# Performance work log

Hardware: AMD Instinct MI355X
Metric: run time of the kernel (lower is better)

## Reference

```python
import jax, jax.numpy as jnp
import numpy as np

N = 50000        # nodes
E = 800000       # edges (avg degree 16)
F_IN = 128       # num_features
DIM = 128        # hidden dim
C = 10           # num_classes
TEMP = 0.6       # EntropyLinear default temperature
SLOPE = 0.01     # F.leaky_relu default negative slope


def setup_inputs() -> dict:
    key = jax.random.key(0)
    ks = jax.random.split(key, 12)
    x = jax.random.normal(ks[0], (N, F_IN), dtype=jnp.float32)
    edge_index = jax.random.randint(ks[1], (2, E), 0, N, dtype=jnp.int32)
    s_in = 1.0 / np.sqrt(F_IN)
    s_d = 1.0 / np.sqrt(DIM)
    W0 = jax.random.normal(ks[2], (F_IN, DIM), jnp.float32) * s_in
    b0 = jnp.zeros((DIM,), jnp.float32)
    W1 = jax.random.normal(ks[3], (DIM, DIM), jnp.float32) * s_d
    b1 = jnp.zeros((DIM,), jnp.float32)
    W2 = jax.random.normal(ks[4], (DIM, DIM), jnp.float32) * s_d
    b2 = jnp.zeros((DIM,), jnp.float32)
    W3 = jax.random.normal(ks[5], (DIM, DIM), jnp.float32) * s_d
    b3 = jnp.zeros((DIM,), jnp.float32)
    lens_w = jax.random.normal(ks[6], (C, 1, DIM), jnp.float32) * s_d  # (n_classes, out=1, in)
    lens_b = jax.random.normal(ks[7], (C, 1, 1), jnp.float32) * 0.01
    return dict(x=x, edge_index=edge_index, W0=W0, b0=b0, W1=W1, b1=b1,
                W2=W2, b2=b2, W3=W3, b3=b3, lens_w=lens_w, lens_b=lens_b)


def _gcn_conv(h, W, b, src, dst, norm):
    # PyG GCNConv: h' = scatter_add( norm_e * (h W)[src] ) + b
    m = h @ W                                  # [N, out]
    msg = m[src] * norm[:, None]               # [E+N, out] gather + scale
    agg = jax.ops.segment_sum(msg, dst, num_segments=N)
    return agg + b


def reference(x, edge_index, W0, b0, W1, b1, W2, b2, W3, b3, lens_w, lens_b):
    loops = jnp.arange(N, dtype=edge_index.dtype)
    src = jnp.concatenate([edge_index[0], loops])   # add self-loops
    dst = jnp.concatenate([edge_index[1], loops])
    deg = jax.ops.segment_sum(jnp.ones_like(dst, jnp.float32), dst, num_segments=N)
    dis = jnp.where(deg > 0, jax.lax.rsqrt(jnp.maximum(deg, 1.0)), 0.0)
    norm = dis[src] * dis[dst]                      # symmetric D^-1/2 A D^-1/2

    h = x
    for W, b in ((W0, b0), (W1, b1), (W2, b2), (W3, b3)):
        h = _gcn_conv(h, W, b, src, dst, norm)
        h = jax.nn.leaky_relu(h, SLOPE)

    p = jax.nn.softmax(h, axis=-1)
    concepts = p / jnp.max(p, axis=-1, keepdims=True)   # [N, DIM]

    # torch_explain EntropyLinear(DIM, 1, n_classes=C)
    gamma = jnp.abs(lens_w).sum(axis=1)                 # [C, DIM] L1 over out_features
    alpha = jax.nn.softmax(gamma / TEMP, axis=1)
    alpha_norm = alpha / jnp.max(alpha, axis=1, keepdims=True)
    z = concepts[None, :, :] * alpha_norm[:, None, :]   # [C, N, DIM]
    out = jnp.einsum('cnd,cod->cno', z, lens_w) + lens_b  # [C, N, 1]
    out = jnp.transpose(out, (1, 0, 2))                 # [N, C, 1]

    log_probs = jax.nn.log_softmax(out, axis=0).squeeze(-1)  # softmax over nodes
    return concepts, log_probs
```

## Files before the change

kernel.cpp:

```cpp
#include <hip/hip_runtime.h>


#define DIMF 128
#define GRID 1024
#define TPB  256

typedef __bf16 bf16x8 __attribute__((ext_vector_type(8)));
typedef float f32x4 __attribute__((ext_vector_type(4)));

static __device__ __forceinline__ ushort f2bf(float f) {
    uint u = __float_as_uint(f);
    u += 0x7fffu + ((u >> 16) & 1u);
    return (ushort)(u >> 16);
}
static __device__ __forceinline__ float bflo(uint u) { return __uint_as_float(u << 16); }
static __device__ __forceinline__ float bfhi(uint u) { return __uint_as_float(u & 0xffff0000u); }

static __device__ __forceinline__ void upadd(float* acc, const int4& u) {
    const uint* w = (const uint*)&u;
#pragma unroll
    for (int k = 0; k < 4; ++k) {
        acc[2 * k]     += bflo(w[k]);
        acc[2 * k + 1] += bfhi(w[k]);
    }
}


union SMem {
    ushort ws[16384];
    struct { int h[256]; } ha;
    struct { int tmp[256]; } sc;
    struct { int h[256]; int lb[256]; } sa;
    struct { int cnt[256]; int cur[256]; int tmp[256]; } pb;
    struct { float wcT[1280]; float lb[16]; } ep;
    struct { float2 red[4]; } r1;
    struct { float red[2]; } wc;
    struct { float2 red2[176]; float Ls[16]; } l3;
};


static __device__ __forceinline__ void gsync(uint* cb, uint r, uint& pop, uint xcc) {
    __syncthreads();
    if (threadIdx.x == 0) {
        uint* axc   = cb + 128 + 32 * xcc;
        uint* xdone = cb + 640 + 32 * xcc;
        uint* root  = cb + 32;
        if (pop == 0) {
            while (__hip_atomic_load(cb, __ATOMIC_RELAXED, __HIP_MEMORY_SCOPE_AGENT) < (uint)GRID)
                __builtin_amdgcn_s_sleep(2);
            pop = __hip_atomic_load(cb + 64 + xcc, __ATOMIC_RELAXED, __HIP_MEMORY_SCOPE_AGENT);
        }
        uint v = __hip_atomic_fetch_add(axc, 1u, __ATOMIC_RELAXED, __HIP_MEMORY_SCOPE_AGENT) + 1;
        if (v == r * pop) {
            __hip_atomic_fetch_add(root, pop, __ATOMIC_RELEASE, __HIP_MEMORY_SCOPE_AGENT);
            while (__hip_atomic_load(root, __ATOMIC_RELAXED, __HIP_MEMORY_SCOPE_AGENT) < r * (uint)GRID)
                __builtin_amdgcn_s_sleep(2);
            asm volatile("buffer_inv\n\tbuffer_inv sc1\n\ts_waitcnt vmcnt(0)" ::: "memory");
            __hip_atomic_store(xdone, r, __ATOMIC_RELAXED, __HIP_MEMORY_SCOPE_AGENT);
        } else {
            while (__hip_atomic_load(xdone, __ATOMIC_RELAXED, __HIP_MEMORY_SCOPE_AGENT) < r)
                __builtin_amdgcn_s_sleep(2);
            asm volatile("buffer_inv\n\ts_waitcnt vmcnt(0)" ::: "memory");
        }
    }
    __syncthreads();
}


static __device__ __forceinline__ void ldws(ushort* ws, const ushort* WTsL, int tid) {
    const int4* src = (const int4*)WTsL;
    int4* dst = (int4*)ws;
#pragma unroll
    for (int i = 0; i < 8; ++i) dst[tid + 256 * i] = src[tid + 256 * i];
}

static __device__ __forceinline__ void mfma_store(const ushort* ws, const int4* a,
        const float* dis, ushort* M, int nrows, int it, int tid) {
    int wave = tid >> 6, lane = tid & 63;
    int lo = lane & 15, hi = lane >> 4;
    f32x4 acc[8];
#pragma unroll
    for (int ct = 0; ct < 8; ++ct) acc[ct] = (f32x4){0.f, 0.f, 0.f, 0.f};
#pragma unroll
    for (int kc = 0; kc < 4; ++kc) {
        bf16x8 av = __builtin_bit_cast(bf16x8, a[kc]);
#pragma unroll
        for (int ct = 0; ct < 8; ++ct) {
            int col = ct * 16 + lo;
            int byte = (col * 256 + kc * 64 + hi * 16) ^ ((col & 7) << 4);
            bf16x8 bv = *(const bf16x8*)((const char*)ws + byte);
            acc[ct] = __builtin_amdgcn_mfma_f32_16x16x32_bf16(av, bv, acc[ct], 0, 0, 0);
        }
    }
    int rbase = it * 64 + wave * 16 + hi * 4;
#pragma unroll
    for (int r = 0; r < 4; ++r) {
        int orow = rbase + r;
        if (orow < nrows) {
            float dn = dis[orow];
#pragma unroll
            for (int ct = 0; ct < 8; ++ct)
                M[((size_t)(ct >> 1) * nrows + orow) * 32 + (ct & 1) * 16 + lo]
                    = f2bf(dn * acc[ct][r]);
        }
    }
}

static __device__ __forceinline__ void gemm_phase(ushort* ws, const ushort* H,
        const ushort* WTsL, const float* dis, ushort* M, int n, int bid, int tid) {
    int nI = (n + 63) >> 6;
    for (int it = bid; it < nI; it += GRID) {
        __syncthreads();
        ldws(ws, WTsL, tid);
        int wave = tid >> 6, lane = tid & 63;
        int lo = lane & 15, hi = lane >> 4;
        int arow = it * 64 + wave * 16 + lo;
        bool inb = arow < n;
        int4 a[4];
        const int4* h4 = (const int4*)H;
#pragma unroll
        for (int kc = 0; kc < 4; ++kc) {
            int4 z = {0, 0, 0, 0};
            a[kc] = inb ? h4[((size_t)kc * n + arow) * 4 + hi] : z;
        }
        __syncthreads();
        mfma_store(ws, a, dis, M, n, it, tid);
    }
}

static __device__ __forceinline__ void gemm0_phase(ushort* ws, const float* X,
        const ushort* WTsL, const float* dis, ushort* M, int n, int bid, int tid) {
    int nI = (n + 63) >> 6;
    for (int it = bid; it < nI; it += GRID) {
        __syncthreads();
        ldws(ws, WTsL, tid);
        int wave = tid >> 6, lane = tid & 63;
        int lo = lane & 15, hi = lane >> 4;
        int arow = it * 64 + wave * 16 + lo;
        bool inb = arow < n;
        int4 a[4];
        const float4* x4 = (const float4*)X;
#pragma unroll
        for (int kc = 0; kc < 4; ++kc) {
            float4 f0 = make_float4(0.f, 0.f, 0.f, 0.f), f1 = f0;
            if (inb) {
                f0 = x4[(size_t)arow * 32 + kc * 8 + hi * 2];
                f1 = x4[(size_t)arow * 32 + kc * 8 + hi * 2 + 1];
            }
            ushort u[8] = { f2bf(f0.x), f2bf(f0.y), f2bf(f0.z), f2bf(f0.w),
                            f2bf(f1.x), f2bf(f1.y), f2bf(f1.z), f2bf(f1.w) };
            a[kc] = *(const int4*)u;
        }
        __syncthreads();
        mfma_store(ws, a, dis, M, n, it, tid);
    }
}


static __device__ __forceinline__ void agg_phase(const int4* Ms4, const ushort* csr,
        const int* offs, const float* dis, const float* bias, int4* Hs4,
        int n, int bid, int tid) {
    int nI = ((n + 63) >> 6) * 4;
    for (int it = bid; it < nI; it += GRID) {
        int slice = it & 3;
        int node = (it >> 2) * 64 + (tid >> 2);
        if (node >= n) continue;
        int q = tid & 3;
        const int4* M = Ms4 + (size_t)slice * n * 4;
        int beg = offs[node], end = offs[node + 1];

        float acc[8];
        {
            int4 u = M[(size_t)node * 4 + q];
            const uint* w = (const uint*)&u;
#pragma unroll
            for (int k = 0; k < 4; ++k) { acc[2 * k] = bflo(w[k]); acc[2 * k + 1] = bfhi(w[k]); }
        }

        int ee = beg;
        for (; ee + 4 <= end; ee += 4) {
            int s0 = csr[ee], s1 = csr[ee + 1], s2 = csr[ee + 2], s3 = csr[ee + 3];
            int4 u0 = M[(size_t)s0 * 4 + q];
            int4 u1 = M[(size_t)s1 * 4 + q];
            int4 u2 = M[(size_t)s2 * 4 + q];
            int4 u3 = M[(size_t)s3 * 4 + q];
            upadd(acc, u0); upadd(acc, u1); upadd(acc, u2); upadd(acc, u3);
        }
        for (; ee < end; ++ee) {
            int4 u0 = M[(size_t)csr[ee] * 4 + q];
            upadd(acc, u0);
        }

        float dn = dis[node];
        const float2* b2 = (const float2*)bias + slice * 16 + q * 4;
        uint o[4];
#pragma unroll
        for (int k = 0; k < 4; ++k) {
            float2 bk = b2[k];
            float v0 = dn * acc[2 * k] + bk.x, v1 = dn * acc[2 * k + 1] + bk.y;
            v0 = v0 > 0.f ? v0 : 0.01f * v0;
            v1 = v1 > 0.f ? v1 : 0.01f * v1;
            o[k] = (uint)f2bf(v0) | ((uint)f2bf(v1) << 16);
        }
        Hs4[(size_t)slice * n * 4 + (size_t)node * 4 + q] = *(const int4*)o;
    }
}


__global__ __launch_bounds__(TPB, 4) void mega_k(
        const float* __restrict__ x, const int* __restrict__ esrc,
        const int* __restrict__ edst,
        const float* __restrict__ W0f, const float* __restrict__ W1f,
        const float* __restrict__ W2f, const float* __restrict__ W3f,
        const float* __restrict__ b0, const float* __restrict__ b1,
        const float* __restrict__ b2, const float* __restrict__ b3,
        const float* __restrict__ lens_w, const float* __restrict__ lens_b,
        uint* cb, int* bcnt, int* gbase, int* gcur, int* offs, float* dis,
        uint* stage, ushort* csr, ushort* mbuf, ushort* hA, ushort* hB,
        ushort* WTs, float* outbuf, float* wcomb, float2* part,
        float* conc, float* logp, int n, int e, int ncls) {
    __shared__ SMem sm;
    const int bid = blockIdx.x;
    const int tid = threadIdx.x;
    const int NB = (n + 255) >> 8;
    const int EB = (e + 1023) >> 10;
    uint rr = 0;

    uint xcc;
    asm volatile("s_getreg_b32 %0, hwreg(HW_REG_XCC_ID)" : "=s"(xcc));
    xcc &= 15;
    uint pop = 0;
    if (tid == 0) {
        __hip_atomic_fetch_add(cb + 64 + xcc, 1u, __ATOMIC_RELAXED, __HIP_MEMORY_SCOPE_AGENT);
        asm volatile("s_waitcnt vmcnt(0)" ::: "memory");
        __hip_atomic_fetch_add(cb, 1u, __ATOMIC_RELAXED, __HIP_MEMORY_SCOPE_AGENT);
    }

    {
        int nI = EB + 256 + ncls;
        for (int it = bid; it < nI; it += GRID) {
            __syncthreads();
            if (it < EB) {
                sm.ha.h[tid] = 0;
                __syncthreads();
                int base = it * 1024;
#pragma unroll
                for (int k = 0; k < 4; ++k) {
                    int i = base + k * 256 + tid;
                    if (i < e) atomicAdd(&sm.ha.h[edst[i] >> 8], 1);
                }
                __syncthreads();
                if (sm.ha.h[tid]) atomicAdd(&bcnt[tid], sm.ha.h[tid]);
            } else if (it < EB + 256) {
                int wi = it - EB;
                const float* W = (wi >= 192) ? W3f : (wi >= 128) ? W2f
                               : (wi >= 64) ? W1f : W0f;
                ushort* outp = WTs + (size_t)(wi >> 6) * 16384;
                int idx = (wi & 63) * 256 + tid;
                int col = idx >> 7, k = idx & 127;
                float w = W[k * 128 + col];
                int byte = ((col * 128 + k) * 2) ^ ((col & 7) << 4);
                *(ushort*)((char*)outp + byte) = f2bf(w);
            } else {
                int c = it - EB - 256;
                float w = 0.f, g = 0.f, m = -1.f;
                if (tid < 128) { w = lens_w[c * 128 + tid]; g = fabsf(w); m = g; }
#pragma unroll
                for (int off = 32; off; off >>= 1) m = fmaxf(m, __shfl_xor(m, off));
                if (tid < 128 && (tid & 63) == 0) sm.wc.red[tid >> 6] = m;
                __syncthreads();
                if (tid < 128) {
                    m = fmaxf(sm.wc.red[0], sm.wc.red[1]);
                    wcomb[c * 128 + tid] = __expf((g - m) * (1.0f / 0.6f)) * w;
                }
            }
        }
    }
    gsync(cb, ++rr, pop, xcc);

    if (bid == 0) {
        int v = (tid < NB) ? bcnt[tid] : 0;
        sm.sc.tmp[tid] = v;
        __syncthreads();
        int run = v;
        for (int off = 1; off < 256; off <<= 1) {
            int a = (tid >= off) ? sm.sc.tmp[tid - off] : 0;
            __syncthreads();
            run += a;
            sm.sc.tmp[tid] = run;
            __syncthreads();
        }
        if (tid < NB) { gbase[tid] = run - v; gcur[tid] = run - v; }
        if (tid == 0) gbase[NB] = e;
    }
    gsync(cb, ++rr, pop, xcc);

    for (int it = bid; it < EB; it += GRID) {
        __syncthreads();
        sm.sa.h[tid] = 0;
        __syncthreads();
        int base = it * 1024;
        int r[4], bk[4];
        uint val[4];
#pragma unroll
        for (int k = 0; k < 4; ++k) {
            int i = base + k * 256 + tid;
            if (i < e) {
                int s = esrc[i], d = edst[i];
                bk[k] = d >> 8;
                val[k] = ((uint)(d & 255) << 16) | (uint)s;
                r[k] = atomicAdd(&sm.sa.h[bk[k]], 1);
            } else bk[k] = -1;
        }
        __syncthreads();
        if (sm.sa.h[tid]) sm.sa.lb[tid] = atomicAdd(&gcur[tid], sm.sa.h[tid]);
        __syncthreads();
#pragma unroll
        for (int k = 0; k < 4; ++k)
            if (bk[k] >= 0) stage[sm.sa.lb[bk[k]] + r[k]] = val[k];
    }
    gsync(cb, ++rr, pop, xcc);

    for (int it = bid; it < NB; it += GRID) {
        __syncthreads();
        int e0 = gbase[it], e1 = gbase[it + 1];
        sm.pb.cnt[tid] = 0;
        __syncthreads();
        for (int i = e0 + tid; i < e1; i += 256) atomicAdd(&sm.pb.cnt[stage[i] >> 16], 1);
        __syncthreads();
        int v = sm.pb.cnt[tid];
        int run = v;
        sm.pb.tmp[tid] = run;
        __syncthreads();
        for (int off = 1; off < 256; off <<= 1) {
            int a = (tid >= off) ? sm.pb.tmp[tid - off] : 0;
            __syncthreads();
            run += a;
            sm.pb.tmp[tid] = run;
            __syncthreads();
        }
        int ex = e0 + run - v;
        int node = it * 256 + tid;
        if (node < n) {
            offs[node] = ex;
            dis[node] = rsqrtf((float)(v + 1));
        }
        sm.pb.cur[tid] = ex;
        __syncthreads();
        for (int i = e0 + tid; i < e1; i += 256) {
            uint w = stage[i];
            int slot = atomicAdd(&sm.pb.cur[w >> 16], 1);
            csr[slot] = (ushort)(w & 0xffffu);
        }
        if (it == 0 && tid == 0) offs[n] = e;
    }
    gsync(cb, ++rr, pop, xcc);

    gemm0_phase(sm.ws, x, WTs, dis, mbuf, n, bid, tid);
    gsync(cb, ++rr, pop, xcc);
    agg_phase((const int4*)mbuf, csr, offs, dis, b0, (int4*)hA, n, bid, tid);
    gsync(cb, ++rr, pop, xcc);
    gemm_phase(sm.ws, hA, WTs + 16384, dis, mbuf, n, bid, tid);
    gsync(cb, ++rr, pop, xcc);
    agg_phase((const int4*)mbuf, csr, offs, dis, b1, (int4*)hB, n, bid, tid);
    gsync(cb, ++rr, pop, xcc);
    gemm_phase(sm.ws, hB, WTs + 2 * 16384, dis, mbuf, n, bid, tid);
    gsync(cb, ++rr, pop, xcc);
    agg_phase((const int4*)mbuf, csr, offs, dis, b2, (int4*)hA, n, bid, tid);
    gsync(cb, ++rr, pop, xcc);
    gemm_phase(sm.ws, hA, WTs + 3 * 16384, dis, mbuf, n, bid, tid);
    gsync(cb, ++rr, pop, xcc);
    agg_phase((const int4*)mbuf, csr, offs, dis, b3, (int4*)hB, n, bid, tid);
    gsync(cb, ++rr, pop, xcc);

    {
        for (int i = tid; i < ncls * 128; i += TPB) {
            int c = i >> 7, d = i & 127;
            sm.ep.wcT[c * 128 + (d & 7) * 16 + (d >> 3)] = wcomb[i];
        }
        if (tid < ncls) sm.ep.lb[tid] = lens_b[tid];
        __syncthreads();
        const int4* Hs4 = (const int4*)hB;
        int nI = (n + 15) >> 4;
        for (int it = bid; it < nI; it += GRID) {
            int node = it * 16 + (tid >> 4);
            if (node >= n) continue;
            int li = tid & 15;
            int slice = li >> 2, q = li & 3;

            int4 u = Hs4[((size_t)slice * n + node) * 4 + q];
            float v[8];
            {
                const uint* w = (const uint*)&u;
#pragma unroll
                for (int k = 0; k < 4; ++k) { v[2 * k] = bflo(w[k]); v[2 * k + 1] = bfhi(w[k]); }
            }
            float m = v[0];
#pragma unroll
            for (int j = 1; j < 8; ++j) m = fmaxf(m, v[j]);
#pragma unroll
            for (int off = 8; off; off >>= 1) m = fmaxf(m, __shfl_xor(m, off));

            float c8[8];
#pragma unroll
            for (int j = 0; j < 8; ++j) c8[j] = __expf(v[j] - m);

            float4* cc = (float4*)(conc + (size_t)node * 128 + li * 8);
            cc[0] = make_float4(c8[0], c8[1], c8[2], c8[3]);
            cc[1] = make_float4(c8[4], c8[5], c8[6], c8[7]);

            for (int c = 0; c < ncls; ++c) {
                float pv = 0.f;
#pragma unroll
                for (int j = 0; j < 8; ++j) pv += c8[j] * sm.ep.wcT[c * 128 + j * 16 + li];
#pragma unroll
                for (int off = 8; off; off >>= 1) pv += __shfl_xor(pv, off);
                if (li == 0) outbuf[(size_t)c * n + node] = pv + sm.ep.lb[c];
            }
        }
    }
    gsync(cb, ++rr, pop, xcc);

    {
        const int nch = 64;
        const int chunk = (n + nch - 1) / nch;
        int nI = nch * ncls;
        for (int it = bid; it < nI; it += GRID) {
            __syncthreads();
            int cx = it & 63, c = it >> 6;
            const float* col = outbuf + (size_t)c * n;
            int i0 = cx * chunk;
            int i1 = min(n, i0 + chunk);
            float m = -3.0e38f, s = 0.f;
            for (int i = i0 + tid; i < i1; i += TPB) {
                float xv = col[i];
                if (xv > m) { s = s * __expf(m - xv) + 1.f; m = xv; }
                else        { s += __expf(xv - m); }
            }
#pragma unroll
            for (int off = 32; off; off >>= 1) {
                float m2 = __shfl_xor(m, off), s2 = __shfl_xor(s, off);
                float mm = fmaxf(m, m2);
                s = s * __expf(m - mm) + s2 * __expf(m2 - mm);
                m = mm;
            }
            int lane = tid & 63, w = tid >> 6;
            if (lane == 0) sm.r1.red[w] = make_float2(m, s);
            __syncthreads();
            if (tid == 0) {
                m = sm.r1.red[0].x; s = sm.r1.red[0].y;
                for (int k = 1; k < 4; ++k) {
                    float m2 = sm.r1.red[k].x, s2 = sm.r1.red[k].y;
                    float mm = fmaxf(m, m2);
                    s = s * __expf(m - mm) + s2 * __expf(m2 - mm);
                    m = mm;
                }
                part[(size_t)c * nch + cx] = make_float2(m, s);
            }
        }
    }
    gsync(cb, ++rr, pop, xcc);

    {
        int c = tid >> 4, j = tid & 15;
        if (tid < ncls * 16) {
            float m = -3.0e38f, s = 0.f;
#pragma unroll
            for (int k = j * 4; k < j * 4 + 4; ++k) {
                float2 pp = part[(size_t)c * 64 + k];
                float mm = fmaxf(m, pp.x);
                s = s * __expf(m - mm) + pp.y * __expf(pp.x - mm);
                m = mm;
            }
            sm.l3.red2[c * 16 + j] = make_float2(m, s);
        }
        __syncthreads();
        if (tid < ncls) {
            float m = -3.0e38f, s = 0.f;
            for (int k = 0; k < 16; ++k) {
                float2 pp = sm.l3.red2[tid * 16 + k];
                float mm = fmaxf(m, pp.x);
                s = s * __expf(m - mm) + pp.y * __expf(pp.x - mm);
                m = mm;
            }
            sm.l3.Ls[tid] = m + __logf(s);
        }
        __syncthreads();
        int nI = (n + 255) >> 8;
        for (int it = bid; it < nI; it += GRID) {
            int i = it * 256 + tid;
            if (i < n)
                for (int c2 = 0; c2 < ncls; ++c2)
                    logp[(size_t)i * ncls + c2] = outbuf[(size_t)c2 * n + i] - sm.l3.Ls[c2];
        }
    }
}


extern "C" void kernel_launch(void* const* d_in, const int* in_sizes, int n_in,
                              void* d_out, int out_size, void* d_ws, size_t ws_size,
                              hipStream_t stream) {
    const int N = in_sizes[0] / DIMF;
    const int E = in_sizes[1] / 2;
    const int C = in_sizes[10] / DIMF;

    const float* x    = (const float*)d_in[0];
    const int*   ei   = (const int*)d_in[1];
    const int*   esrc = ei;
    const int*   edst = ei + E;
    const float* W0 = (const float*)d_in[2];
    const float* W1 = (const float*)d_in[4];
    const float* W2 = (const float*)d_in[6];
    const float* W3 = (const float*)d_in[8];
    const float* b0 = (const float*)d_in[3];
    const float* b1 = (const float*)d_in[5];
    const float* b2 = (const float*)d_in[7];
    const float* b3 = (const float*)d_in[9];
    const float* lens_w = (const float*)d_in[10];
    const float* lens_b = (const float*)d_in[11];

    float* out_concepts = (float*)d_out;
    float* out_logp     = (float*)d_out + (size_t)N * DIMF;

    char* p = (char*)d_ws;
    auto alloc = [&](size_t bytes) -> void* {
        void* r = (void*)p;
        p += (bytes + 255) & ~(size_t)255;
        return r;
    };
    uint*   cb     = (uint*)alloc(8192);
    int*    bcnt   = (int*)alloc(256 * 4);
    int*    gbase  = (int*)alloc(257 * 4);
    int*    gcur   = (int*)alloc(256 * 4);
    int*    offs   = (int*)alloc(((size_t)N + 1) * 4);
    float*  dis    = (float*)alloc((size_t)N * 4);
    uint*   stage  = (uint*)alloc((size_t)E * 4);
    ushort* csr    = (ushort*)alloc((size_t)E * 2);
    ushort* mbuf   = (ushort*)alloc((size_t)N * DIMF * 2);
    ushort* hA     = (ushort*)alloc((size_t)N * DIMF * 2);
    ushort* hB     = (ushort*)alloc((size_t)N * DIMF * 2);
    ushort* WTs    = (ushort*)alloc((size_t)4 * 16384 * 2);
    float*  outbuf = (float*)alloc((size_t)C * N * 4);
    float*  wcomb  = (float*)alloc((size_t)C * DIMF * 4);
    float2* part   = (float2*)alloc((size_t)C * 64 * 8);

    hipMemsetAsync(cb, 0, 8192 + 1024, stream);

    mega_k<<<GRID, TPB, 0, stream>>>(
        x, esrc, edst, W0, W1, W2, W3, b0, b1, b2, b3, lens_w, lens_b,
        cb, bcnt, gbase, gcur, offs, dis, stage, csr, mbuf, hA, hB,
        WTs, outbuf, wcomb, part, out_concepts, out_logp, N, E, C);
}
```

Baseline: 285.2 us.

## Split GEMM weight tiles into column halves to raise persistent-grid occupancy

The per-block weight staging in shared memory is halved by processing 64 output columns per work item instead of 128, so each GEMM row tile becomes two work items. This shrinks the LDS union from 32KB to 16KB, which allows 7 blocks per CU, and the persistent grid grows from 1024 to 1792 blocks. The cost is that A rows are loaded twice, and the grid-wide barrier now has more participants, which may add overhead to every phase sync.

```diff
diff --git a/kernel.cpp b/kernel.cpp
--- a/kernel.cpp
+++ b/kernel.cpp
@@ -2,7 +2,7 @@
 
 
 #define DIMF 128
-#define GRID 1024
+#define GRID 1792
 #define TPB  256
 
 typedef __bf16 bf16x8 __attribute__((ext_vector_type(8)));
@@ -27,7 +27,7 @@
 
 
 union SMem {
-    ushort ws[16384];
+    ushort ws[8192];
     struct { int h[256]; } ha;
     struct { int tmp[256]; } sc;
     struct { int h[256]; int lb[256]; } sa;
@@ -67,54 +67,58 @@
 }
 
 
-static __device__ __forceinline__ void ldws(ushort* ws, const ushort* WTsL, int tid) {
-    const int4* src = (const int4*)WTsL;
+static __device__ __forceinline__ void ldws_half(ushort* ws, const ushort* WTsL,
+                                                 int ch, int tid) {
+    const int4* src = (const int4*)(WTsL + ch * 8192);
     int4* dst = (int4*)ws;
 #pragma unroll
-    for (int i = 0; i < 8; ++i) dst[tid + 256 * i] = src[tid + 256 * i];
-}
-
-static __device__ __forceinline__ void mfma_store(const ushort* ws, const int4* a,
-        const float* dis, ushort* M, int nrows, int it, int tid) {
+    for (int i = 0; i < 4; ++i) dst[tid + 256 * i] = src[tid + 256 * i];
+}
+
+static __device__ __forceinline__ void mfma_store_half(const ushort* ws, const int4* a,
+        const float* dis, ushort* M, int nrows, int rt, int ch, int tid) {
     int wave = tid >> 6, lane = tid & 63;
     int lo = lane & 15, hi = lane >> 4;
-    f32x4 acc[8];
-#pragma unroll
-    for (int ct = 0; ct < 8; ++ct) acc[ct] = (f32x4){0.f, 0.f, 0.f, 0.f};
+    f32x4 acc[4];
+#pragma unroll
+    for (int ct = 0; ct < 4; ++ct) acc[ct] = (f32x4){0.f, 0.f, 0.f, 0.f};
 #pragma unroll
     for (int kc = 0; kc < 4; ++kc) {
         bf16x8 av = __builtin_bit_cast(bf16x8, a[kc]);
 #pragma unroll
-        for (int ct = 0; ct < 8; ++ct) {
+        for (int ct = 0; ct < 4; ++ct) {
             int col = ct * 16 + lo;
             int byte = (col * 256 + kc * 64 + hi * 16) ^ ((col & 7) << 4);
             bf16x8 bv = *(const bf16x8*)((const char*)ws + byte);
             acc[ct] = __builtin_amdgcn_mfma_f32_16x16x32_bf16(av, bv, acc[ct], 0, 0, 0);
         }
     }
-    int rbase = it * 64 + wave * 16 + hi * 4;
+    int rbase = rt * 64 + wave * 16 + hi * 4;
 #pragma unroll
     for (int r = 0; r < 4; ++r) {
         int orow = rbase + r;
         if (orow < nrows) {
             float dn = dis[orow];
 #pragma unroll
-            for (int ct = 0; ct < 8; ++ct)
-                M[((size_t)(ct >> 1) * nrows + orow) * 32 + (ct & 1) * 16 + lo]
+            for (int ct = 0; ct < 4; ++ct) {
+                int g = ch * 4 + ct;
+                M[((size_t)(g >> 1) * nrows + orow) * 32 + (g & 1) * 16 + lo]
                     = f2bf(dn * acc[ct][r]);
+            }
         }
     }
 }
 
 static __device__ __forceinline__ void gemm_phase(ushort* ws, const ushort* H,
         const ushort* WTsL, const float* dis, ushort* M, int n, int bid, int tid) {
-    int nI = (n + 63) >> 6;
+    int nI = ((n + 63) >> 6) * 2;
     for (int it = bid; it < nI; it += GRID) {
-        __syncthreads();
-        ldws(ws, WTsL, tid);
+        int rt = it >> 1, ch = it & 1;
+        __syncthreads();
+        ldws_half(ws, WTsL, ch, tid);
         int wave = tid >> 6, lane = tid & 63;
         int lo = lane & 15, hi = lane >> 4;
-        int arow = it * 64 + wave * 16 + lo;
+        int arow = rt * 64 + wave * 16 + lo;
         bool inb = arow < n;
         int4 a[4];
         const int4* h4 = (const int4*)H;
@@ -124,19 +128,20 @@
             a[kc] = inb ? h4[((size_t)kc * n + arow) * 4 + hi] : z;
         }
         __syncthreads();
-        mfma_store(ws, a, dis, M, n, it, tid);
+        mfma_store_half(ws, a, dis, M, n, rt, ch, tid);
     }
 }
 
 static __device__ __forceinline__ void gemm0_phase(ushort* ws, const float* X,
         const ushort* WTsL, const float* dis, ushort* M, int n, int bid, int tid) {
-    int nI = (n + 63) >> 6;
+    int nI = ((n + 63) >> 6) * 2;
     for (int it = bid; it < nI; it += GRID) {
-        __syncthreads();
-        ldws(ws, WTsL, tid);
+        int rt = it >> 1, ch = it & 1;
+        __syncthreads();
+        ldws_half(ws, WTsL, ch, tid);
         int wave = tid >> 6, lane = tid & 63;
         int lo = lane & 15, hi = lane >> 4;
-        int arow = it * 64 + wave * 16 + lo;
+        int arow = rt * 64 + wave * 16 + lo;
         bool inb = arow < n;
         int4 a[4];
         const float4* x4 = (const float4*)X;
@@ -152,7 +157,7 @@
             a[kc] = *(const int4*)u;
         }
         __syncthreads();
-        mfma_store(ws, a, dis, M, n, it, tid);
+        mfma_store_half(ws, a, dis, M, n, rt, ch, tid);
     }
 }
 
@@ -207,7 +212,7 @@
 }
 
 
-__global__ __launch_bounds__(TPB, 4) void mega_k(
+__global__ __launch_bounds__(TPB, 7) void mega_k(
         const float* __restrict__ x, const int* __restrict__ esrc,
         const int* __restrict__ edst,
         const float* __restrict__ W0f, const float* __restrict__ W1f,
```

Measured after the change: 310.4 us. +8.8%, slower.

## Split persistent megakernel into three kernels with smaller LDS and larger grid

Applied to the files above, without the earlier changes.

Splits the single persistent cooperative kernel into three kernels (CSR build, GCN layers, tail) that each have their own smaller shared-memory footprint, and raises the grid from 1024 to 1792 blocks. The layer GEMM now stages the weight matrix in two 16KB halves instead of one 32KB tile, so more blocks can be resident per CU (launch bounds 7-8). The aim is higher occupancy for the latency-bound gather aggregation. In exchange it adds two kernel launches, extra barriers in the GEMM, and more blocks taking part in each software grid barrier, which relies on all 1792 blocks being co-resident.

```diff
diff --git a/kernel.cpp b/kernel.cpp
--- a/kernel.cpp
+++ b/kernel.cpp
@@ -2,7 +2,7 @@
 
 
 #define DIMF 128
-#define GRID 1024
+#define GRID 1792
 #define TPB  256
 
 typedef __bf16 bf16x8 __attribute__((ext_vector_type(8)));
@@ -26,29 +26,28 @@
 }
 
 
-union SMem {
-    ushort ws[16384];
-    struct { int h[256]; } ha;
-    struct { int tmp[256]; } sc;
-    struct { int h[256]; int lb[256]; } sa;
-    struct { int cnt[256]; int cur[256]; int tmp[256]; } pb;
-    struct { float wcT[1280]; float lb[16]; } ep;
-    struct { float2 red[4]; } r1;
-    struct { float red[2]; } wc;
-    struct { float2 red2[176]; float Ls[16]; } l3;
-};
-
-
-static __device__ __forceinline__ void gsync(uint* cb, uint r, uint& pop, uint xcc) {
+static __device__ __forceinline__ uint reg_xcd(uint* cbk, int tid) {
+    uint xcc;
+    asm volatile("s_getreg_b32 %0, hwreg(HW_REG_XCC_ID)" : "=s"(xcc));
+    xcc &= 15;
+    if (tid == 0) {
+        __hip_atomic_fetch_add(cbk + 64 + xcc, 1u, __ATOMIC_RELAXED, __HIP_MEMORY_SCOPE_AGENT);
+        asm volatile("s_waitcnt vmcnt(0)" ::: "memory");
+        __hip_atomic_fetch_add(cbk, 1u, __ATOMIC_RELAXED, __HIP_MEMORY_SCOPE_AGENT);
+    }
+    return xcc;
+}
+
+static __device__ __forceinline__ void gsync(uint* cbk, uint r, uint& pop, uint xcc) {
     __syncthreads();
     if (threadIdx.x == 0) {
-        uint* axc   = cb + 128 + 32 * xcc;
-        uint* xdone = cb + 640 + 32 * xcc;
-        uint* root  = cb + 32;
+        uint* axc   = cbk + 128 + 32 * xcc;
+        uint* xdone = cbk + 640 + 32 * xcc;
+        uint* root  = cbk + 32;
         if (pop == 0) {
-            while (__hip_atomic_load(cb, __ATOMIC_RELAXED, __HIP_MEMORY_SCOPE_AGENT) < (uint)GRID)
+            while (__hip_atomic_load(cbk, __ATOMIC_RELAXED, __HIP_MEMORY_SCOPE_AGENT) < (uint)GRID)
                 __builtin_amdgcn_s_sleep(2);
-            pop = __hip_atomic_load(cb + 64 + xcc, __ATOMIC_RELAXED, __HIP_MEMORY_SCOPE_AGENT);
+            pop = __hip_atomic_load(cbk + 64 + xcc, __ATOMIC_RELAXED, __HIP_MEMORY_SCOPE_AGENT);
         }
         uint v = __hip_atomic_fetch_add(axc, 1u, __ATOMIC_RELAXED, __HIP_MEMORY_SCOPE_AGENT) + 1;
         if (v == r * pop) {
@@ -67,174 +66,30 @@
 }
 
 
-static __device__ __forceinline__ void ldws(ushort* ws, const ushort* WTsL, int tid) {
-    const int4* src = (const int4*)WTsL;
-    int4* dst = (int4*)ws;
-#pragma unroll
-    for (int i = 0; i < 8; ++i) dst[tid + 256 * i] = src[tid + 256 * i];
-}
-
-static __device__ __forceinline__ void mfma_store(const ushort* ws, const int4* a,
-        const float* dis, ushort* M, int nrows, int it, int tid) {
-    int wave = tid >> 6, lane = tid & 63;
-    int lo = lane & 15, hi = lane >> 4;
-    f32x4 acc[8];
-#pragma unroll
-    for (int ct = 0; ct < 8; ++ct) acc[ct] = (f32x4){0.f, 0.f, 0.f, 0.f};
-#pragma unroll
-    for (int kc = 0; kc < 4; ++kc) {
-        bf16x8 av = __builtin_bit_cast(bf16x8, a[kc]);
-#pragma unroll
-        for (int ct = 0; ct < 8; ++ct) {
-            int col = ct * 16 + lo;
-            int byte = (col * 256 + kc * 64 + hi * 16) ^ ((col & 7) << 4);
-            bf16x8 bv = *(const bf16x8*)((const char*)ws + byte);
-            acc[ct] = __builtin_amdgcn_mfma_f32_16x16x32_bf16(av, bv, acc[ct], 0, 0, 0);
-        }
-    }
-    int rbase = it * 64 + wave * 16 + hi * 4;
-#pragma unroll
-    for (int r = 0; r < 4; ++r) {
-        int orow = rbase + r;
-        if (orow < nrows) {
-            float dn = dis[orow];
-#pragma unroll
-            for (int ct = 0; ct < 8; ++ct)
-                M[((size_t)(ct >> 1) * nrows + orow) * 32 + (ct & 1) * 16 + lo]
-                    = f2bf(dn * acc[ct][r]);
-        }
-    }
-}
-
-static __device__ __forceinline__ void gemm_phase(ushort* ws, const ushort* H,
-        const ushort* WTsL, const float* dis, ushort* M, int n, int bid, int tid) {
-    int nI = (n + 63) >> 6;
-    for (int it = bid; it < nI; it += GRID) {
-        __syncthreads();
-        ldws(ws, WTsL, tid);
-        int wave = tid >> 6, lane = tid & 63;
-        int lo = lane & 15, hi = lane >> 4;
-        int arow = it * 64 + wave * 16 + lo;
-        bool inb = arow < n;
-        int4 a[4];
-        const int4* h4 = (const int4*)H;
-#pragma unroll
-        for (int kc = 0; kc < 4; ++kc) {
-            int4 z = {0, 0, 0, 0};
-            a[kc] = inb ? h4[((size_t)kc * n + arow) * 4 + hi] : z;
-        }
-        __syncthreads();
-        mfma_store(ws, a, dis, M, n, it, tid);
-    }
-}
-
-static __device__ __forceinline__ void gemm0_phase(ushort* ws, const float* X,
-        const ushort* WTsL, const float* dis, ushort* M, int n, int bid, int tid) {
-    int nI = (n + 63) >> 6;
-    for (int it = bid; it < nI; it += GRID) {
-        __syncthreads();
-        ldws(ws, WTsL, tid);
-        int wave = tid >> 6, lane = tid & 63;
-        int lo = lane & 15, hi = lane >> 4;
-        int arow = it * 64 + wave * 16 + lo;
-        bool inb = arow < n;
-        int4 a[4];
-        const float4* x4 = (const float4*)X;
-#pragma unroll
-        for (int kc = 0; kc < 4; ++kc) {
-            float4 f0 = make_float4(0.f, 0.f, 0.f, 0.f), f1 = f0;
-            if (inb) {
-                f0 = x4[(size_t)arow * 32 + kc * 8 + hi * 2];
-                f1 = x4[(size_t)arow * 32 + kc * 8 + hi * 2 + 1];
-            }
-            ushort u[8] = { f2bf(f0.x), f2bf(f0.y), f2bf(f0.z), f2bf(f0.w),
-                            f2bf(f1.x), f2bf(f1.y), f2bf(f1.z), f2bf(f1.w) };
-            a[kc] = *(const int4*)u;
-        }
-        __syncthreads();
-        mfma_store(ws, a, dis, M, n, it, tid);
-    }
-}
-
-
-static __device__ __forceinline__ void agg_phase(const int4* Ms4, const ushort* csr,
-        const int* offs, const float* dis, const float* bias, int4* Hs4,
-        int n, int bid, int tid) {
-    int nI = ((n + 63) >> 6) * 4;
-    for (int it = bid; it < nI; it += GRID) {
-        int slice = it & 3;
-        int node = (it >> 2) * 64 + (tid >> 2);
-        if (node >= n) continue;
-        int q = tid & 3;
-        const int4* M = Ms4 + (size_t)slice * n * 4;
-        int beg = offs[node], end = offs[node + 1];
-
-        float acc[8];
-        {
-            int4 u = M[(size_t)node * 4 + q];
-            const uint* w = (const uint*)&u;
-#pragma unroll
-            for (int k = 0; k < 4; ++k) { acc[2 * k] = bflo(w[k]); acc[2 * k + 1] = bfhi(w[k]); }
-        }
-
-        int ee = beg;
-        for (; ee + 4 <= end; ee += 4) {
-            int s0 = csr[ee], s1 = csr[ee + 1], s2 = csr[ee + 2], s3 = csr[ee + 3];
-            int4 u0 = M[(size_t)s0 * 4 + q];
-            int4 u1 = M[(size_t)s1 * 4 + q];
-            int4 u2 = M[(size_t)s2 * 4 + q];
-            int4 u3 = M[(size_t)s3 * 4 + q];
-            upadd(acc, u0); upadd(acc, u1); upadd(acc, u2); upadd(acc, u3);
-        }
-        for (; ee < end; ++ee) {
-            int4 u0 = M[(size_t)csr[ee] * 4 + q];
-            upadd(acc, u0);
-        }
-
-        float dn = dis[node];
-        const float2* b2 = (const float2*)bias + slice * 16 + q * 4;
-        uint o[4];
-#pragma unroll
-        for (int k = 0; k < 4; ++k) {
-            float2 bk = b2[k];
-            float v0 = dn * acc[2 * k] + bk.x, v1 = dn * acc[2 * k + 1] + bk.y;
-            v0 = v0 > 0.f ? v0 : 0.01f * v0;
-            v1 = v1 > 0.f ? v1 : 0.01f * v1;
-            o[k] = (uint)f2bf(v0) | ((uint)f2bf(v1) << 16);
-        }
-        Hs4[(size_t)slice * n * 4 + (size_t)node * 4 + q] = *(const int4*)o;
-    }
-}
-
-
-__global__ __launch_bounds__(TPB, 4) void mega_k(
-        const float* __restrict__ x, const int* __restrict__ esrc,
-        const int* __restrict__ edst,
+union SMemA {
+    struct { int h[256]; } ha;
+    struct { int tmp[256]; } sc;
+    struct { int h[256]; int lb[256]; } sa;
+    struct { int cnt[256]; int cur[256]; int tmp[256]; } pb;
+    struct { float red[2]; } wc;
+};
+
+__global__ __launch_bounds__(TPB, 8) void csr_k(
+        const int* __restrict__ esrc, const int* __restrict__ edst,
         const float* __restrict__ W0f, const float* __restrict__ W1f,
         const float* __restrict__ W2f, const float* __restrict__ W3f,
-        const float* __restrict__ b0, const float* __restrict__ b1,
-        const float* __restrict__ b2, const float* __restrict__ b3,
-        const float* __restrict__ lens_w, const float* __restrict__ lens_b,
-        uint* cb, int* bcnt, int* gbase, int* gcur, int* offs, float* dis,
-        uint* stage, ushort* csr, ushort* mbuf, ushort* hA, ushort* hB,
-        ushort* WTs, float* outbuf, float* wcomb, float2* part,
-        float* conc, float* logp, int n, int e, int ncls) {
-    __shared__ SMem sm;
+        const float* __restrict__ lens_w,
+        uint* cbk, int* bcnt, int* gbase, int* gcur, int* offs, float* dis,
+        uint* stage, ushort* csr, ushort* WTs, float* wcomb,
+        int n, int e, int ncls) {
+    __shared__ SMemA sm;
     const int bid = blockIdx.x;
     const int tid = threadIdx.x;
     const int NB = (n + 255) >> 8;
     const int EB = (e + 1023) >> 10;
     uint rr = 0;
-
-    uint xcc;
-    asm volatile("s_getreg_b32 %0, hwreg(HW_REG_XCC_ID)" : "=s"(xcc));
-    xcc &= 15;
+    uint xcc = reg_xcd(cbk, tid);
     uint pop = 0;
-    if (tid == 0) {
-        __hip_atomic_fetch_add(cb + 64 + xcc, 1u, __ATOMIC_RELAXED, __HIP_MEMORY_SCOPE_AGENT);
-        asm volatile("s_waitcnt vmcnt(0)" ::: "memory");
-        __hip_atomic_fetch_add(cb, 1u, __ATOMIC_RELAXED, __HIP_MEMORY_SCOPE_AGENT);
-    }
 
     {
         int nI = EB + 256 + ncls;
@@ -276,7 +131,7 @@
             }
         }
     }
-    gsync(cb, ++rr, pop, xcc);
+    gsync(cbk, ++rr, pop, xcc);
 
     if (bid == 0) {
         int v = (tid < NB) ? bcnt[tid] : 0;
@@ -293,7 +148,7 @@
         if (tid < NB) { gbase[tid] = run - v; gcur[tid] = run - v; }
         if (tid == 0) gbase[NB] = e;
     }
-    gsync(cb, ++rr, pop, xcc);
+    gsync(cbk, ++rr, pop, xcc);
 
     for (int it = bid; it < EB; it += GRID) {
         __syncthreads();
@@ -319,7 +174,7 @@
         for (int k = 0; k < 4; ++k)
             if (bk[k] >= 0) stage[sm.sa.lb[bk[k]] + r[k]] = val[k];
     }
-    gsync(cb, ++rr, pop, xcc);
+    gsync(cbk, ++rr, pop, xcc);
 
     for (int it = bid; it < NB; it += GRID) {
         __syncthreads();
@@ -354,24 +209,198 @@
         }
         if (it == 0 && tid == 0) offs[n] = e;
     }
-    gsync(cb, ++rr, pop, xcc);
-
-    gemm0_phase(sm.ws, x, WTs, dis, mbuf, n, bid, tid);
-    gsync(cb, ++rr, pop, xcc);
+}
+
+
+static __device__ __forceinline__ void ldws_half(ushort* ws, const ushort* WTsL,
+                                                 int ch, int tid) {
+    const int4* src = (const int4*)(WTsL + ch * 8192);
+    int4* dst = (int4*)ws;
+#pragma unroll
+    for (int i = 0; i < 4; ++i) dst[tid + 256 * i] = src[tid + 256 * i];
+}
+
+static __device__ __forceinline__ void gemm_body(ushort* ws, const ushort* WTsL,
+        const int4* a, const float* dis, ushort* M, int n, int it, int tid) {
+    int wave = tid >> 6, lane = tid & 63;
+    int lo = lane & 15, hi = lane >> 4;
+    f32x4 acc[8];
+#pragma unroll
+    for (int ct = 0; ct < 8; ++ct) acc[ct] = (f32x4){0.f, 0.f, 0.f, 0.f};
+#pragma unroll
+    for (int ch = 0; ch < 2; ++ch) {
+        __syncthreads();
+        ldws_half(ws, WTsL, ch, tid);
+        __syncthreads();
+#pragma unroll
+        for (int kc = 0; kc < 4; ++kc) {
+            bf16x8 av = __builtin_bit_cast(bf16x8, a[kc]);
+#pragma unroll
+            for (int ct = 0; ct < 4; ++ct) {
+                int col = ct * 16 + lo;
+                int byte = (col * 256 + kc * 64 + hi * 16) ^ ((col & 7) << 4);
+                bf16x8 bv = *(const bf16x8*)((const char*)ws + byte);
+                acc[ch * 4 + ct] =
+                    __builtin_amdgcn_mfma_f32_16x16x32_bf16(av, bv, acc[ch * 4 + ct], 0, 0, 0);
+            }
+        }
+    }
+    int rbase = it * 64 + wave * 16 + hi * 4;
+#pragma unroll
+    for (int r = 0; r < 4; ++r) {
+        int orow = rbase + r;
+        if (orow < n) {
+            float dn = dis[orow];
+#pragma unroll
+            for (int g = 0; g < 8; ++g)
+                M[((size_t)(g >> 1) * n + orow) * 32 + (g & 1) * 16 + lo]
+                    = f2bf(dn * acc[g][r]);
+        }
+    }
+}
+
+static __device__ __forceinline__ void gemm_phase(ushort* ws, const ushort* H,
+        const ushort* WTsL, const float* dis, ushort* M, int n, int bid, int tid) {
+    int nI = (n + 63) >> 6;
+    for (int it = bid; it < nI; it += GRID) {
+        int wave = tid >> 6, lane = tid & 63;
+        int lo = lane & 15, hi = lane >> 4;
+        int arow = it * 64 + wave * 16 + lo;
+        bool inb = arow < n;
+        int4 a[4];
+        const int4* h4 = (const int4*)H;
+#pragma unroll
+        for (int kc = 0; kc < 4; ++kc) {
+            int4 z = {0, 0, 0, 0};
+            a[kc] = inb ? h4[((size_t)kc * n + arow) * 4 + hi] : z;
+        }
+        gemm_body(ws, WTsL, a, dis, M, n, it, tid);
+    }
+}
+
+static __device__ __forceinline__ void gemm0_phase(ushort* ws, const float* X,
+        const ushort* WTsL, const float* dis, ushort* M, int n, int bid, int tid) {
+    int nI = (n + 63) >> 6;
+    for (int it = bid; it < nI; it += GRID) {
+        int wave = tid >> 6, lane = tid & 63;
+        int lo = lane & 15, hi = lane >> 4;
+        int arow = it * 64 + wave * 16 + lo;
+        bool inb = arow < n;
+        int4 a[4];
+        const float4* x4 = (const float4*)X;
+#pragma unroll
+        for (int kc = 0; kc < 4; ++kc) {
+            float4 f0 = make_float4(0.f, 0.f, 0.f, 0.f), f1 = f0;
+            if (inb) {
+                f0 = x4[(size_t)arow * 32 + kc * 8 + hi * 2];
+                f1 = x4[(size_t)arow * 32 + kc * 8 + hi * 2 + 1];
+            }
+            ushort u[8] = { f2bf(f0.x), f2bf(f0.y), f2bf(f0.z), f2bf(f0.w),
+                            f2bf(f1.x), f2bf(f1.y), f2bf(f1.z), f2bf(f1.w) };
+            a[kc] = *(const int4*)u;
+        }
+        gemm_body(ws, WTsL, a, dis, M, n, it, tid);
+    }
+}
+
+static __device__ __forceinline__ void agg_phase(const int4* Ms4, const ushort* csr,
+        const int* offs, const float* dis, const float* bias, int4* Hs4,
+        int n, int bid, int tid) {
+    int nI = ((n + 63) >> 6) * 4;
+    for (int it = bid; it < nI; it += GRID) {
+        int slice = it & 3;
+        int node = (it >> 2) * 64 + (tid >> 2);
+        if (node >= n) continue;
+        int q = tid & 3;
+        const int4* M = Ms4 + (size_t)slice * n * 4;
+        int beg = offs[node], end = offs[node + 1];
+
+        float acc[8];
+        {
+            int4 u = M[(size_t)node * 4 + q];
+            const uint* w = (const uint*)&u;
+#pragma unroll
+            for (int k = 0; k < 4; ++k) { acc[2 * k] = bflo(w[k]); acc[2 * k + 1] = bfhi(w[k]); }
+        }
+
+        int ee = beg;
+        for (; ee + 4 <= end; ee += 4) {
+            int s0 = csr[ee], s1 = csr[ee + 1], s2 = csr[ee + 2], s3 = csr[ee + 3];
+            int4 u0 = M[(size_t)s0 * 4 + q];
+            int4 u1 = M[(size_t)s1 * 4 + q];
+            int4 u2 = M[(size_t)s2 * 4 + q];
+            int4 u3 = M[(size_t)s3 * 4 + q];
+            upadd(acc, u0); upadd(acc, u1); upadd(acc, u2); upadd(acc, u3);
+        }
+        for (; ee < end; ++ee) {
+            int4 u0 = M[(size_t)csr[ee] * 4 + q];
+            upadd(acc, u0);
+        }
+
+        float dn = dis[node];
+        const float2* b2 = (const float2*)bias + slice * 16 + q * 4;
+        uint o[4];
+#pragma unroll
+        for (int k = 0; k < 4; ++k) {
+            float2 bk = b2[k];
+            float v0 = dn * acc[2 * k] + bk.x, v1 = dn * acc[2 * k + 1] + bk.y;
+            v0 = v0 > 0.f ? v0 : 0.01f * v0;
+            v1 = v1 > 0.f ? v1 : 0.01f * v1;
+            o[k] = (uint)f2bf(v0) | ((uint)f2bf(v1) << 16);
+        }
+        Hs4[(size_t)slice * n * 4 + (size_t)node * 4 + q] = *(const int4*)o;
+    }
+}
+
+__global__ __launch_bounds__(TPB, 7) void layers_k(
+        const float* __restrict__ x,
+        const float* __restrict__ b0, const float* __restrict__ b1,
+        const float* __restrict__ b2, const float* __restrict__ b3,
+        uint* cbk, const int* __restrict__ offs, const float* __restrict__ dis,
+        const ushort* __restrict__ csr, ushort* mbuf, ushort* hA, ushort* hB,
+        const ushort* __restrict__ WTs, int n) {
+    __shared__ ushort ws[8192];
+    const int bid = blockIdx.x;
+    const int tid = threadIdx.x;
+    uint rr = 0;
+    uint xcc = reg_xcd(cbk, tid);
+    uint pop = 0;
+
+    gemm0_phase(ws, x, WTs, dis, mbuf, n, bid, tid);
+    gsync(cbk, ++rr, pop, xcc);
     agg_phase((const int4*)mbuf, csr, offs, dis, b0, (int4*)hA, n, bid, tid);
-    gsync(cb, ++rr, pop, xcc);
-    gemm_phase(sm.ws, hA, WTs + 16384, dis, mbuf, n, bid, tid);
-    gsync(cb, ++rr, pop, xcc);
+    gsync(cbk, ++rr, pop, xcc);
+    gemm_phase(ws, hA, WTs + 16384, dis, mbuf, n, bid, tid);
+    gsync(cbk, ++rr, pop, xcc);
     agg_phase((const int4*)mbuf, csr, offs, dis, b1, (int4*)hB, n, bid, tid);
-    gsync(cb, ++rr, pop, xcc);
-    gemm_phase(sm.ws, hB, WTs + 2 * 16384, dis, mbuf, n, bid, tid);
-    gsync(cb, ++rr, pop, xcc);
+    gsync(cbk, ++rr, pop, xcc);
+    gemm_phase(ws, hB, WTs + 2 * 16384, dis, mbuf, n, bid, tid);
+    gsync(cbk, ++rr, pop, xcc);
     agg_phase((const int4*)mbuf, csr, offs, dis, b2, (int4*)hA, n, bid, tid);
-    gsync(cb, ++rr, pop, xcc);
-    gemm_phase(sm.ws, hA, WTs + 3 * 16384, dis, mbuf, n, bid, tid);
-    gsync(cb, ++rr, pop, xcc);
+    gsync(cbk, ++rr, pop, xcc);
+    gemm_phase(ws, hA, WTs + 3 * 16384, dis, mbuf, n, bid, tid);
+    gsync(cbk, ++rr, pop, xcc);
     agg_phase((const int4*)mbuf, csr, offs, dis, b3, (int4*)hB, n, bid, tid);
-    gsync(cb, ++rr, pop, xcc);
+}
+
+
+union SMemC {
+    struct { float wcT[1280]; float lb[16]; } ep;
+    struct { float2 red[4]; } r1;
+    struct { float2 red2[176]; float Ls[16]; } l3;
+};
+
+__global__ __launch_bounds__(TPB, 8) void tail_k(
+        const float* __restrict__ lens_b,
+        uint* cbk, const ushort* __restrict__ hB,
+        const float* __restrict__ wcomb, float* outbuf, float2* part,
+        float* conc, float* logp, int n, int ncls) {
+    __shared__ SMemC sm;
+    const int bid = blockIdx.x;
+    const int tid = threadIdx.x;
+    uint rr = 0;
+    uint xcc = reg_xcd(cbk, tid);
+    uint pop = 0;
 
     {
         for (int i = tid; i < ncls * 128; i += TPB) {
@@ -419,7 +448,7 @@
             }
         }
     }
-    gsync(cb, ++rr, pop, xcc);
+    gsync(cbk, ++rr, pop, xcc);
 
     {
         const int nch = 64;
@@ -459,7 +488,7 @@
             }
         }
     }
-    gsync(cb, ++rr, pop, xcc);
+    gsync(cbk, ++rr, pop, xcc);
 
     {
         int c = tid >> 4, j = tid & 15;
@@ -528,7 +557,7 @@
         p += (bytes + 255) & ~(size_t)255;
         return r;
     };
-    uint*   cb     = (uint*)alloc(8192);
+    uint*   cb     = (uint*)alloc(3 * 8192);
     int*    bcnt   = (int*)alloc(256 * 4);
     int*    gbase  = (int*)alloc(257 * 4);
     int*    gcur   = (int*)alloc(256 * 4);
@@ -544,10 +573,17 @@
     float*  wcomb  = (float*)alloc((size_t)C * DIMF * 4);
     float2* part   = (float2*)alloc((size_t)C * 64 * 8);
 
-    hipMemsetAsync(cb, 0, 8192 + 1024, stream);
-
-    mega_k<<<GRID, TPB, 0, stream>>>(
-        x, esrc, edst, W0, W1, W2, W3, b0, b1, b2, b3, lens_w, lens_b,
-        cb, bcnt, gbase, gcur, offs, dis, stage, csr, mbuf, hA, hB,
-        WTs, outbuf, wcomb, part, out_concepts, out_logp, N, E, C);
-}
+    hipMemsetAsync(cb, 0, 3 * 8192 + 1024, stream);
+
+    uint* cbA = cb;
+    uint* cbB = cb + 2048;
+    uint* cbC = cb + 4096;
+
+    csr_k<<<GRID, TPB, 0, stream>>>(esrc, edst, W0, W1, W2, W3, lens_w,
+                                    cbA, bcnt, gbase, gcur, offs, dis,
+                                    stage, csr, WTs, wcomb, N, E, C);
+    layers_k<<<GRID, TPB, 0, stream>>>(x, b0, b1, b2, b3,
+                                       cbB, offs, dis, csr, mbuf, hA, hB, WTs, N);
+    tail_k<<<GRID, TPB, 0, stream>>>(lens_b, cbC, hB, wcomb, outbuf, part,
+                                     out_concepts, out_logp, N, C);
+}
```

New measurement: 376.3 us. 1.32x slower.
